# Optimization experiments

Measured on AMD Instinct MI355X. Metric: run time of the kernel, lower is better.

## Reference

```python
import jax, jax.numpy as jnp
import numpy as np

L, E, S, H, D, V = 6, 384, 256, 6, 64, 65
FF = 4 * E


def _ln(x, g, b, ddof, eps=1e-5):
    mean = jnp.mean(x, axis=-1, keepdims=True)
    var = jnp.var(x, axis=-1, keepdims=True, ddof=ddof)
    return g * (x - mean) / jnp.sqrt(var + eps) + b


def setup_inputs() -> dict:
    key = jax.random.key(0)
    ks = jax.random.split(key, 16)
    std = 0.02
    inp = {
        'x': jax.random.randint(ks[0], (64, S), 0, V),
        'tok_emb': jax.random.normal(ks[1], (V, E)) * std,
        'pos_emb': jax.random.normal(ks[2], (S, E)) * std,
        'Wq': jax.random.normal(ks[3], (L, E, H * D)) * std,
        'Wk': jax.random.normal(ks[4], (L, E, H * D)) * std,
        'Wv': jax.random.normal(ks[5], (L, E, H * D)) * std,
        'Wproj': jax.random.normal(ks[6], (L, H * D, E)) * std,
        'bproj': jnp.zeros((L, E)),
        'W1': jax.random.normal(ks[7], (L, E, FF)) * std,
        'b1': jnp.zeros((L, FF)),
        'W2': jax.random.normal(ks[8], (L, FF, E)) * std,
        'b2': jnp.zeros((L, E)),
        'ln1_g': jnp.ones((L, E)), 'ln1_b': jnp.zeros((L, E)),
        'ln2_g': jnp.ones((L, E)), 'ln2_b': jnp.zeros((L, E)),
        'lnf_g': jnp.ones((E,)), 'lnf_b': jnp.zeros((E,)),
        'Wlm': jax.random.normal(ks[9], (E, V)) * std,
        'blm': jnp.zeros((V,)),
    }
    return inp


def _forward(x, tok_emb, pos_emb, Wq, Wk, Wv, Wproj, bproj, W1, b1, W2, b2,
             ln1_g, ln1_b, ln2_g, ln2_b, lnf_g, lnf_b, Wlm, blm):
    B, T = x.shape
    h = tok_emb[x] + pos_emb[:T]  # [B,T,E]
    causal = jnp.tril(jnp.ones((T, T), dtype=bool))
    neg_inf = jnp.finfo(h.dtype).min
    for l in range(L):
        hn = _ln(h, ln1_g[l], ln1_b[l], ddof=1)  # custom LayerNorm uses unbiased var
        q = (hn @ Wq[l]).reshape(B, T, H, D)
        k = (hn @ Wk[l]).reshape(B, T, H, D)
        v = (hn @ Wv[l]).reshape(B, T, H, D)
        wei = jnp.einsum('bqhd,bkhd->bhqk', q, k) * (D ** -0.5)
        wei = jnp.where(causal, wei, neg_inf)
        wei = jax.nn.softmax(wei, axis=-1)
        att = jnp.einsum('bhqk,bkhd->bqhd', wei, v).reshape(B, T, H * D)
        h = h + att @ Wproj[l] + bproj[l]
        hn = _ln(h, ln2_g[l], ln2_b[l], ddof=1)
        h = h + jax.nn.relu(hn @ W1[l] + b1[l]) @ W2[l] + b2[l]
    h = _ln(h, lnf_g, lnf_b, ddof=0)  # nn.LayerNorm uses biased var
    return h @ Wlm + blm  # logits [B,T,V]


def reference(x, tok_emb, pos_emb, Wq, Wk, Wv, Wproj, bproj, W1, b1, W2, b2,
              ln1_g, ln1_b, ln2_g, ln2_b, lnf_g, lnf_b, Wlm, blm):
    return _forward(x, tok_emb, pos_emb, Wq, Wk, Wv, Wproj, bproj, W1, b1, W2, b2,
                    ln1_g, ln1_b, ln2_g, ln2_b, lnf_g, lnf_b, Wlm, blm)
```

## Files before the change

kernel.cpp:

```cpp
#include <hip/hip_runtime.h>

#define L_  6
#define E_  384
#define T_  256
#define H_  6
#define D_  64
#define V_  65
#define FF_ 1536
#define B_  64
#define BT_ (B_*T_)
#define HD_ 384

typedef __attribute__((ext_vector_type(8))) short short8;
typedef __attribute__((ext_vector_type(4))) float f32x4;
typedef unsigned short us;
typedef unsigned int u32;

__device__ __forceinline__ us f2bf(float f) {
  u32 u = __float_as_uint(f);
  u32 r = (u + 0x7fffu + ((u >> 16) & 1u)) >> 16;
  return (us)r;
}
__device__ __forceinline__ float bf2f(us v) {
  return __uint_as_float(((u32)v) << 16);
}

__device__ __forceinline__ int xcd_swz(int b, int nwg) {
  const int q = nwg >> 3;
  return (b & 7) * q + (b >> 3);
}

__global__ void embed_kernel(const int* __restrict__ x, const float* __restrict__ tok,
                             const float* __restrict__ pos, us* __restrict__ h) {
  const int total8 = BT_ * E_ / 8;
  for (int i = blockIdx.x * blockDim.x + threadIdx.x; i < total8;
       i += gridDim.x * blockDim.x) {
    const int flat = i << 3;
    const int row  = flat / E_;
    const int e    = flat - row * E_;
    const int id   = x[row];
    const float4 a0 = *reinterpret_cast<const float4*>(tok + id * E_ + e);
    const float4 a1 = *reinterpret_cast<const float4*>(tok + id * E_ + e + 4);
    const float4 p0 = *reinterpret_cast<const float4*>(pos + (row & (T_ - 1)) * E_ + e);
    const float4 p1 = *reinterpret_cast<const float4*>(pos + (row & (T_ - 1)) * E_ + e + 4);
    short8 o;
    o[0] = (short)f2bf(a0.x + p0.x); o[1] = (short)f2bf(a0.y + p0.y);
    o[2] = (short)f2bf(a0.z + p0.z); o[3] = (short)f2bf(a0.w + p0.w);
    o[4] = (short)f2bf(a1.x + p1.x); o[5] = (short)f2bf(a1.y + p1.y);
    o[6] = (short)f2bf(a1.z + p1.z); o[7] = (short)f2bf(a1.w + p1.w);
    *reinterpret_cast<short8*>(h + flat) = o;
  }
}

template<int DDOF>
__global__ __launch_bounds__(512)
void stats_kernel(const us* __restrict__ h, float2* __restrict__ st) {
  const int wave = threadIdx.x >> 6;
  const int lane = threadIdx.x & 63;
  const int row  = (blockIdx.x << 3) + wave;
  float sum = 0.f, sq = 0.f;
  if (lane < 48) {
    const short8 v = *reinterpret_cast<const short8*>(h + (size_t)row * E_ + lane * 8);
#pragma unroll
    for (int j = 0; j < 8; ++j) {
      const float f = bf2f((us)v[j]);
      sum += f; sq += f * f;
    }
  }
#pragma unroll
  for (int off = 32; off > 0; off >>= 1) {
    sum += __shfl_xor(sum, off);
    sq  += __shfl_xor(sq, off);
  }
  if (lane == 0) {
    const float mean = sum * (1.f / E_);
    const float var  = (sq - E_ * mean * mean) * (1.f / (E_ - DDOF));
    float2 o; o.x = mean; o.y = rsqrtf(var + 1e-5f);
    st[row] = o;
  }
}

__global__ void prep_kernel(const float* __restrict__ Wq, const float* __restrict__ Wk,
                            const float* __restrict__ Wv, const float* __restrict__ Wpr,
                            const float* __restrict__ W1, const float* __restrict__ W2,
                            const float* __restrict__ Wlm,
                            us* qkvT, us* projT, us* W1T, us* W2T, us* WlmT,
                            const float* __restrict__ ln1g,
                            const float* __restrict__ ln2g,
                            const float* __restrict__ lnfg) {
  const int t = blockIdx.x;
  const float* src; us* dst; const float* g = nullptr;
  int K, N, Ndst, bx, by;
  if (t < 2592) {
    const int z = t / 144, rem = t % 144;
    bx = rem % 12; by = rem / 12;
    const int sel = z / 6, l = z % 6;
    src = (sel == 0 ? Wq : sel == 1 ? Wk : Wv) + (size_t)l * 147456;
    dst = qkvT + (size_t)l * 442368 + sel * 147456;
    g = ln1g + l * 384; K = 384; N = 384; Ndst = 384;
  } else if (t < 3456) {
    const int t2 = t - 2592, l = t2 / 144, rem = t2 % 144;
    bx = rem % 12; by = rem / 12;
    src = Wpr + (size_t)l * 147456; dst = projT + (size_t)l * 147456;
    K = 384; N = 384; Ndst = 384;
  } else if (t < 6912) {
    const int t3 = t - 3456, l = t3 / 576, rem = t3 % 576;
    bx = rem % 48; by = rem / 48;
    src = W1 + (size_t)l * 589824; dst = W1T + (size_t)l * 589824;
    g = ln2g + l * 384; K = 384; N = 1536; Ndst = 1536;
  } else if (t < 10368) {
    const int t4 = t - 6912, l = t4 / 576, rem = t4 % 576;
    bx = rem % 12; by = rem / 12;
    src = W2 + (size_t)l * 589824; dst = W2T + (size_t)l * 589824;
    K = 1536; N = 384; Ndst = 384;
  } else {
    const int t5 = t - 10368;
    bx = t5 % 4; by = t5 / 4;
    src = Wlm; dst = WlmT; g = lnfg; K = 384; N = 65; Ndst = 128;
  }
  __shared__ float tt[32][33];
  const int n0 = bx << 5, k0 = by << 5;
  const int tx = threadIdx.x & 31, ty = threadIdx.x >> 5;
#pragma unroll
  for (int j = 0; j < 32; j += 8) {
    const int n = n0 + tx;
    tt[ty + j][tx] = (n < N) ? src[(size_t)(k0 + ty + j) * N + n] : 0.f;
  }
  __syncthreads();
  const float gk = g ? g[k0 + tx] : 1.f;
#pragma unroll
  for (int j = 0; j < 32; j += 8) {
    const int n = n0 + ty + j;
    if (n < Ndst) dst[(size_t)n * K + k0 + tx] = f2bf(tt[tx][ty + j] * gk);
  }
}

__global__ void c12_all(const float* __restrict__ Wq, const float* __restrict__ Wk,
                        const float* __restrict__ Wv, const float* __restrict__ W1,
                        const float* __restrict__ Wlm,
                        const float* __restrict__ ln1g, const float* __restrict__ ln1b,
                        const float* __restrict__ ln2g, const float* __restrict__ ln2b,
                        const float* __restrict__ lnfg, const float* __restrict__ lnfb,
                        float2* c12q, float2* c12f, float2* c12lm) {
  const int t = blockIdx.x;
  const float* Wz; const float* gz; const float* bz; float2* outb; int N, nb;
  if (t < 108) {
    const int bx = t % 6, zy = t / 6, sel = zy / 6, l = zy % 6;
    Wz = (sel == 0 ? Wq : sel == 1 ? Wk : Wv) + (size_t)l * 147456;
    gz = ln1g + l * 384; bz = ln1b + l * 384;
    outb = c12q + (size_t)l * 1152 + sel * 384; N = 384; nb = bx << 6;
  } else if (t < 252) {
    const int t2 = t - 108, bx = t2 % 24, l = t2 / 24;
    Wz = W1 + (size_t)l * 589824;
    gz = ln2g + l * 384; bz = ln2b + l * 384;
    outb = c12f + (size_t)l * 1536; N = 1536; nb = bx << 6;
  } else {
    const int bx = t - 252;
    Wz = Wlm; gz = lnfg; bz = lnfb;
    outb = c12lm; N = 65; nb = bx << 6;
  }
  __shared__ float p1[4][64], p2[4][64];
  const int tt = threadIdx.x;
  const int c = tt & 63, kq = tt >> 6;
  const int n = nb + c;
  float s1 = 0.f, s2 = 0.f;
  if (n < N) {
    for (int k = kq * 96; k < kq * 96 + 96; ++k) {
      const float w = Wz[(size_t)k * N + n];
      s1 = fmaf(gz[k], w, s1);
      s2 = fmaf(bz[k], w, s2);
    }
  }
  p1[kq][c] = s1; p2[kq][c] = s2;
  __syncthreads();
  if (tt < 64 && nb + tt < N) {
    float2 o;
    o.x = p1[0][tt] + p1[1][tt] + p1[2][tt] + p1[3][tt];
    o.y = p2[0][tt] + p2[1][tt] + p2[2][tt] + p2[3][tt];
    outb[nb + tt] = o;
  }
}

template<int ROWS, int CHPR, int NTH>
__device__ __forceinline__ void stageG(const us* g, int rowUs, us* lds, int tid) {
#pragma unroll
  for (int j = 0; j < ROWS * CHPR / NTH; ++j) {
    const int fl  = j * NTH + tid;
    const int row = fl / CHPR;
    const int c   = fl % CHPR;
    const int gc  = (CHPR == 8) ? (c ^ (row & 7)) : (c ^ ((row >> 1) & 3));
    const us* src = g + (size_t)row * rowUs + gc * 8;
    __builtin_amdgcn_global_load_lds(
        (const __attribute__((address_space(1))) u32*)src,
        (__attribute__((address_space(3))) u32*)(lds + ((fl >> 6) << 9)),
        16, 0, 0);
  }
}

#define GEMM_LOOP(K_, NT_)                                                        \
  const int NT = (NT_);                                                           \
  _Pragma("unroll")                                                               \
  for (int p = 0; p < BUFS - 1; ++p) {                                            \
    stageG<BM, 4, 256>(Abase + p * 32, (K_), As[p], tid);                         \
    stageG<BN, 4, 256>(Bbase + p * 32, (K_), Bs[p], tid);                         \
  }                                                                               \
  int cb = 0;                                                                     \
  for (int t = 0; t < NT; ++t) {                                                  \
    if constexpr (BUFS == 4) {                                                    \
      if (t < NT - 2)       asm volatile("s_waitcnt vmcnt(%0)" :: "n"(2 * LPS) : "memory"); \
      else if (t == NT - 2) asm volatile("s_waitcnt vmcnt(%0)" :: "n"(LPS) : "memory");     \
      else                  asm volatile("s_waitcnt vmcnt(0)" ::: "memory");      \
    } else {                                                                      \
      if (t < NT - 1)       asm volatile("s_waitcnt vmcnt(%0)" :: "n"(LPS) : "memory");     \
      else                  asm volatile("s_waitcnt vmcnt(0)" ::: "memory");      \
    }                                                                             \
    __builtin_amdgcn_s_barrier();                                                 \
    __builtin_amdgcn_sched_barrier(0);                                            \
    if (t + BUFS - 1 < NT) {                                                      \
      int ib = cb + (BUFS - 1); if (ib >= BUFS) ib -= BUFS;                       \
      stageG<BM, 4, 256>(Abase + (t + BUFS - 1) * 32, (K_), As[ib], tid);         \
      stageG<BN, 4, 256>(Bbase + (t + BUFS - 1) * 32, (K_), Bs[ib], tid);         \
    }                                                                             \
    short8 af[FM], bfr[FN];                                                       \
    _Pragma("unroll")                                                             \
    for (int mt = 0; mt < FM; ++mt) {                                             \
      const int row = wm + mt * 16 + fm;                                          \
      af[mt] = *(const short8*)(As[cb] + row * 32 + ((fg ^ ((row >> 1) & 3)) << 3)); \
    }                                                                             \
    _Pragma("unroll")                                                             \
    for (int nt = 0; nt < FN; ++nt) {                                             \
      const int row = wn + nt * 16 + fm;                                          \
      bfr[nt] = *(const short8*)(Bs[cb] + row * 32 + ((fg ^ ((row >> 1) & 3)) << 3)); \
    }                                                                             \
    __builtin_amdgcn_s_setprio(1);                                                \
    _Pragma("unroll")                                                             \
    for (int mt = 0; mt < FM; ++mt)                                               \
      _Pragma("unroll")                                                           \
      for (int nt = 0; nt < FN; ++nt)                                             \
        acc[mt][nt] = __builtin_amdgcn_mfma_f32_16x16x32_bf16(af[mt], bfr[nt], acc[mt][nt], 0, 0, 0); \
    __builtin_amdgcn_s_setprio(0);                                                \
    cb = (cb + 1 == BUFS) ? 0 : cb + 1;                                           \
  }

template<int FM, int FN, int BUFS>
__global__ __launch_bounds__(256)
void gemm_mfma(const us* __restrict__ A, const us* __restrict__ Bt,
               const float* __restrict__ bias, const us* Res,
               us* __restrict__ O, int N, int K, int gx) {
  constexpr int BM = FM * 32, BN = FN * 32;
  constexpr int LPS = (BM + BN) * 4 / 256;
  __shared__ us As[BUFS][BM * 32];
  __shared__ us Bs[BUFS][BN * 32];
  const int tid = threadIdx.x;
  const int lid = xcd_swz(blockIdx.x, gridDim.x);
  const int bnI = lid % gx, bmI = lid / gx;
  const int bm = bmI * BM, bn = bnI * BN;
  const int wv = tid >> 6, ln = tid & 63;
  const int fm = ln & 15, fg = ln >> 4;
  const int wm = (wv >> 1) * (FM * 16), wn = (wv & 1) * (FN * 16);
  const us* Abase = A + (size_t)bm * K;
  const us* Bbase = Bt + (size_t)bn * K;

  f32x4 acc[FM][FN];
  const f32x4 zz = {0.f, 0.f, 0.f, 0.f};
#pragma unroll
  for (int i = 0; i < FM; ++i)
#pragma unroll
    for (int j = 0; j < FN; ++j) acc[i][j] = zz;

  GEMM_LOOP(K, K >> 5)

#pragma unroll
  for (int mt = 0; mt < FM; ++mt) {
#pragma unroll
    for (int nt = 0; nt < FN; ++nt) {
      const int col  = bn + wn + nt * 16 + fm;
      const int row0 = bm + wm + mt * 16 + fg * 4;
      const float bc = bias[col];
#pragma unroll
      for (int r = 0; r < 4; ++r) {
        const size_t idx = (size_t)(row0 + r) * N + col;
        O[idx] = f2bf(acc[mt][nt][r] + bc + bf2f(Res[idx]));
      }
    }
  }
}

template<int FM, int FN, int EPI, int BUFS>
__global__ __launch_bounds__(256)
void gemm_fold(const us* __restrict__ A, const us* __restrict__ Bt,
               const float2* __restrict__ st, const float2* __restrict__ c12,
               const float* __restrict__ bias, void* O0, void* O1,
               int N, int gx) {
  constexpr int K = 384;
  constexpr int BM = FM * 32, BN = FN * 32;
  constexpr int LPS = (BM + BN) * 4 / 256;
  __shared__ us As[BUFS][BM * 32];
  __shared__ us Bs[BUFS][BN * 32];
  const int tid = threadIdx.x;
  const int lid = xcd_swz(blockIdx.x, gridDim.x);
  const int bnI = lid % gx, bmI = lid / gx;
  const int bm = bmI * BM, bn = bnI * BN;
  const int wv = tid >> 6, ln = tid & 63;
  const int fm = ln & 15, fg = ln >> 4;
  const int wm = (wv >> 1) * (FM * 16), wn = (wv & 1) * (FN * 16);
  const us* Abase = A + (size_t)bm * K;
  const us* Bbase = Bt + (size_t)bn * K;

  f32x4 acc[FM][FN];
  const f32x4 zz = {0.f, 0.f, 0.f, 0.f};
#pragma unroll
  for (int i = 0; i < FM; ++i)
#pragma unroll
    for (int j = 0; j < FN; ++j) acc[i][j] = zz;

  GEMM_LOOP(K, 12)

#pragma unroll
  for (int mt = 0; mt < FM; ++mt) {
    const int row0 = bm + wm + mt * 16 + fg * 4;
    float2 sr[4];
#pragma unroll
    for (int r = 0; r < 4; ++r) sr[r] = st[row0 + r];
#pragma unroll
    for (int nt = 0; nt < FN; ++nt) {
      const int col = bn + wn + nt * 16 + fm;
      if (EPI == 3 && col >= V_) continue;
      const float2 cc = c12[col];
      float vals[4];
#pragma unroll
      for (int r = 0; r < 4; ++r)
        vals[r] = sr[r].y * (acc[mt][nt][r] - sr[r].x * cc.x) + cc.y;
      if (EPI == 0) {
        if (col < 768) {
          us* qk = (us*)O0;
#pragma unroll
          for (int r = 0; r < 4; ++r)
            qk[(size_t)(row0 + r) * 768 + col] = f2bf(vals[r]);
        } else {
          const int d = col - 768;
          const int hh = d >> 6, dd = d & 63;
          const int bI = row0 >> 8, t0 = row0 & 255;
          us* vt = (us*)O1;
          ushort4 pk;
          pk.x = f2bf(vals[0]); pk.y = f2bf(vals[1]);
          pk.z = f2bf(vals[2]); pk.w = f2bf(vals[3]);
          *reinterpret_cast<ushort4*>(vt + ((size_t)((bI * H_ + hh) * 64 + dd)) * 256 + t0) = pk;
        }
      } else if (EPI == 2) {
        us* o = (us*)O0;
        const float bc = bias[col];
#pragma unroll
        for (int r = 0; r < 4; ++r)
          o[(size_t)(row0 + r) * N + col] = f2bf(fmaxf(vals[r] + bc, 0.f));
      } else {
        float* o = (float*)O0;
        const float bc = bias[col];
#pragma unroll
        for (int r = 0; r < 4; ++r)
          o[(size_t)(row0 + r) * V_ + col] = vals[r] + bc;
      }
    }
  }
}

__global__ __launch_bounds__(256)
void attn_mfma(const us* __restrict__ qk, const us* __restrict__ vT,
               us* __restrict__ ab) {
  __shared__ us Ks[2][64 * 64];
  __shared__ us Vs[2][64 * 64];
  __shared__ us Plds[4][16 * 72];
  const int tid = threadIdx.x, w = tid >> 6, l = tid & 63;
  const int m = l & 15, g = l >> 4;
  const int bi = xcd_swz(blockIdx.x, gridDim.x);
  const int b = bi / 12, rem = bi - b * 12, h = rem >> 1, p = rem & 1;
  const us* Kg = qk + (size_t)(b << 8) * 768 + 384 + h * 64;
  const us* Vg = vT + (size_t)(b * H_ + h) * 64 * 256;

  int cur = 0;
  const f32x4 zz = {0.f, 0.f, 0.f, 0.f};

#pragma unroll
  for (int half = 0; half < 2; ++half) {
    const int qt = half == 0 ? p : 3 - p;
    const int qrow = (b << 8) + (qt << 6) + (w << 4);

    short8 qf0, qf1;
    {
      const us* qp = qk + (size_t)(qrow + m) * 768 + h * 64 + g * 8;
      qf0 = *(const short8*)qp;
      qf1 = *(const short8*)(qp + 32);
    }
    float mrow[4], ssum[4];
    f32x4 o[4];
#pragma unroll
    for (int r = 0; r < 4; ++r) { mrow[r] = -1e30f; ssum[r] = 0.f; o[r] = zz; }

    stageG<64, 8, 256>(Kg, 768, Ks[cur], tid);
    stageG<64, 8, 256>(Vg, 256, Vs[cur], tid);
    __syncthreads();

    for (int kt = 0; kt <= qt; ++kt) {
      if (kt < qt) {
        stageG<64, 8, 256>(Kg + (size_t)(kt + 1) * 64 * 768, 768, Ks[cur ^ 1], tid);
        stageG<64, 8, 256>(Vg + (kt + 1) * 64,               256, Vs[cur ^ 1], tid);
      }
      f32x4 s[4];
      __builtin_amdgcn_s_setprio(1);
#pragma unroll
      for (int nt = 0; nt < 4; ++nt) {
        const int row = nt * 16 + m;
        const int sw  = row & 7;
        short8 kf0 = *(const short8*)(Ks[cur] + row * 64 + ((g ^ sw) << 3));
        short8 kf1 = *(const short8*)(Ks[cur] + row * 64 + (((4 | g) ^ sw) << 3));
        f32x4 z = zz;
        z = __builtin_amdgcn_mfma_f32_16x16x32_bf16(qf0, kf0, z, 0, 0, 0);
        z = __builtin_amdgcn_mfma_f32_16x16x32_bf16(qf1, kf1, z, 0, 0, 0);
        s[nt] = z;
      }
      __builtin_amdgcn_s_setprio(0);
      const bool diag = (kt == qt);
      float pr[4][4], tmax[4];
#pragma unroll
      for (int r = 0; r < 4; ++r) tmax[r] = -1e30f;
#pragma unroll
      for (int nt = 0; nt < 4; ++nt)
#pragma unroll
        for (int r = 0; r < 4; ++r) {
          float v = s[nt][r] * 0.125f;
          if (diag) {
            const int key = nt * 16 + m;
            const int qq  = (w << 4) + (g << 2) + r;
            if (key > qq) v = -1e30f;
          }
          pr[nt][r] = v;
          tmax[r] = fmaxf(tmax[r], v);
        }
#pragma unroll
      for (int xm = 1; xm < 16; xm <<= 1)
#pragma unroll
        for (int r = 0; r < 4; ++r) tmax[r] = fmaxf(tmax[r], __shfl_xor(tmax[r], xm));
      float sc[4], tsum[4];
#pragma unroll
      for (int r = 0; r < 4; ++r) {
        const float nm = fmaxf(mrow[r], tmax[r]);
        sc[r] = __expf(mrow[r] - nm);
        mrow[r] = nm;
        tsum[r] = 0.f;
      }
#pragma unroll
      for (int nt = 0; nt < 4; ++nt)
#pragma unroll
        for (int r = 0; r < 4; ++r) {
          pr[nt][r] = __expf(pr[nt][r] - mrow[r]);
          tsum[r] += pr[nt][r];
        }
#pragma unroll
      for (int xm = 1; xm < 16; xm <<= 1)
#pragma unroll
        for (int r = 0; r < 4; ++r) tsum[r] += __shfl_xor(tsum[r], xm);
#pragma unroll
      for (int r = 0; r < 4; ++r) ssum[r] = ssum[r] * sc[r] + tsum[r];
#pragma unroll
      for (int nt = 0; nt < 4; ++nt)
#pragma unroll
        for (int r = 0; r < 4; ++r) o[nt][r] *= sc[r];
#pragma unroll
      for (int nt = 0; nt < 4; ++nt)
#pragma unroll
        for (int r = 0; r < 4; ++r)
          Plds[w][(g * 4 + r) * 72 + nt * 16 + m] = f2bf(pr[nt][r]);
      __builtin_amdgcn_s_setprio(1);
#pragma unroll
      for (int kc = 0; kc < 2; ++kc) {
        short8 pa = *(const short8*)&Plds[w][m * 72 + kc * 32 + g * 8];
#pragma unroll
        for (int nd = 0; nd < 4; ++nd) {
          const int row = nd * 16 + m;
          short8 vf = *(const short8*)(Vs[cur] + row * 64 + ((((kc << 2) | g) ^ (row & 7)) << 3));
          o[nd] = __builtin_amdgcn_mfma_f32_16x16x32_bf16(pa, vf, o[nd], 0, 0, 0);
        }
      }
      __builtin_amdgcn_s_setprio(0);
      __syncthreads();
      cur ^= 1;
    }
#pragma unroll
    for (int r = 0; r < 4; ++r) {
      const float inv = 1.f / ssum[r];
      const size_t rowoff = (size_t)(qrow + g * 4 + r) * 384 + h * 64;
#pragma unroll
      for (int nd = 0; nd < 4; ++nd)
        ab[rowoff + nd * 16 + m] = f2bf(o[nd][r] * inv);
    }
  }
}

extern "C" void kernel_launch(void* const* d_in, const int* in_sizes, int n_in,
                              void* d_out, int out_size, void* d_ws, size_t ws_size,
                              hipStream_t stream) {
  const int*   x    = (const int*)  d_in[0];
  const float* tok  = (const float*)d_in[1];
  const float* pos  = (const float*)d_in[2];
  const float* Wq   = (const float*)d_in[3];
  const float* Wk   = (const float*)d_in[4];
  const float* Wv   = (const float*)d_in[5];
  const float* Wpr  = (const float*)d_in[6];
  const float* bpr  = (const float*)d_in[7];
  const float* W1   = (const float*)d_in[8];
  const float* b1   = (const float*)d_in[9];
  const float* W2   = (const float*)d_in[10];
  const float* b2   = (const float*)d_in[11];
  const float* ln1g = (const float*)d_in[12];
  const float* ln1b = (const float*)d_in[13];
  const float* ln2g = (const float*)d_in[14];
  const float* ln2b = (const float*)d_in[15];
  const float* lnfg = (const float*)d_in[16];
  const float* lnfb = (const float*)d_in[17];
  const float* Wlm  = (const float*)d_in[18];
  const float* blm  = (const float*)d_in[19];
  float* out = (float*)d_out;

  char* W = (char*)d_ws;
  us*     h    = (us*)(W + 0);
  us*     qkb  = (us*)(W + 12582912);
  us*     vTb  = (us*)(W + 37748736);
  us*     abb  = (us*)(W + 50331648);
  us*     ffa  = (us*)(W + 12582912);
  us*     qkvT = (us*)(W + 62914560);
  us*     projT= (us*)(W + 68222976);
  us*     W1T  = (us*)(W + 69992448);
  us*     W2T  = (us*)(W + 77070336);
  us*     WlmT = (us*)(W + 84148224);
  float2* st   = (float2*)(W + 84246528);
  float2* c12q = (float2*)(W + 84377600);
  float2* c12f = (float2*)(W + 84432896);
  float2* c12lm= (float2*)(W + 84506624);

  prep_kernel<<<10416, 256, 0, stream>>>(Wq, Wk, Wv, Wpr, W1, W2, Wlm,
                                         qkvT, projT, W1T, W2T, WlmT,
                                         ln1g, ln2g, lnfg);
  c12_all<<<254, 256, 0, stream>>>(Wq, Wk, Wv, W1, Wlm,
                                   ln1g, ln1b, ln2g, ln2b, lnfg, lnfb,
                                   c12q, c12f, c12lm);

  embed_kernel<<<3072, 256, 0, stream>>>(x, tok, pos, h);

  for (int l = 0; l < L_; ++l) {
    stats_kernel<1><<<BT_/8, 512, 0, stream>>>(h, st);
    gemm_fold<4,4,0,3><<<1152, 256, 0, stream>>>(
        h, qkvT + (size_t)l*442368, st, c12q + (size_t)l*1152, nullptr,
        qkb, vTb, 1152, 9);
    attn_mfma<<<B_*H_*2, 256, 0, stream>>>(qkb, vTb, abb);
    gemm_mfma<2,4,4><<<768, 256, 0, stream>>>(
        abb, projT + (size_t)l*147456, bpr + l*E_, h, h, 384, 384, 3);
    stats_kernel<1><<<BT_/8, 512, 0, stream>>>(h, st);
    gemm_fold<4,4,2,3><<<1536, 256, 0, stream>>>(
        h, W1T + (size_t)l*589824, st, c12f + (size_t)l*1536, b1 + l*FF_,
        ffa, nullptr, 1536, 12);
    gemm_mfma<2,4,4><<<768, 256, 0, stream>>>(
        ffa, W2T + (size_t)l*589824, b2 + l*E_, h, h, 384, 1536, 3);
  }

  stats_kernel<0><<<BT_/8, 512, 0, stream>>>(h, st);
  gemm_fold<2,4,3,3><<<256, 256, 0, stream>>>(
      h, WlmT, st, c12lm, blm, out, nullptr, 128, 1);
}
```

Before: 876.1 us.

## Share K/V tile loads between both query tiles in causal attention

The attention kernel used to walk the key/value tiles twice, once per query tile in its balanced pair. It now keeps both query tiles' softmax state live and walks the K/V tiles once, so each staged tile feeds both query tiles until the shorter one hits its diagonal. This cuts global K/V loads and barriers for the shorter tile, at the cost of more live registers (two sets of accumulators and running stats), which may lower occupancy.

```diff
diff --git a/kernel.cpp b/kernel.cpp
--- a/kernel.cpp
+++ b/kernel.cpp
@@ -374,125 +374,139 @@
   const int m = l & 15, g = l >> 4;
   const int bi = xcd_swz(blockIdx.x, gridDim.x);
   const int b = bi / 12, rem = bi - b * 12, h = rem >> 1, p = rem & 1;
+  const int qtA = 3 - p, qtB = p;
+  const int qrowA = (b << 8) + (qtA << 6) + (w << 4);
+  const int qrowB = (b << 8) + (qtB << 6) + (w << 4);
   const us* Kg = qk + (size_t)(b << 8) * 768 + 384 + h * 64;
   const us* Vg = vT + (size_t)(b * H_ + h) * 64 * 256;
 
+  short8 qA0, qA1, qB0, qB1;
+  {
+    const us* qp = qk + (size_t)(qrowA + m) * 768 + h * 64 + g * 8;
+    qA0 = *(const short8*)qp;
+    qA1 = *(const short8*)(qp + 32);
+    const us* qp2 = qk + (size_t)(qrowB + m) * 768 + h * 64 + g * 8;
+    qB0 = *(const short8*)qp2;
+    qB1 = *(const short8*)(qp2 + 32);
+  }
+  const f32x4 zz = {0.f, 0.f, 0.f, 0.f};
+  float mrowA[4], ssumA[4], mrowB[4], ssumB[4];
+  f32x4 oA[4], oB[4];
+#pragma unroll
+  for (int r = 0; r < 4; ++r) {
+    mrowA[r] = -1e30f; ssumA[r] = 0.f; oA[r] = zz;
+    mrowB[r] = -1e30f; ssumB[r] = 0.f; oB[r] = zz;
+  }
+
   int cur = 0;
-  const f32x4 zz = {0.f, 0.f, 0.f, 0.f};
-
-#pragma unroll
-  for (int half = 0; half < 2; ++half) {
-    const int qt = half == 0 ? p : 3 - p;
-    const int qrow = (b << 8) + (qt << 6) + (w << 4);
-
-    short8 qf0, qf1;
-    {
-      const us* qp = qk + (size_t)(qrow + m) * 768 + h * 64 + g * 8;
-      qf0 = *(const short8*)qp;
-      qf1 = *(const short8*)(qp + 32);
-    }
-    float mrow[4], ssum[4];
-    f32x4 o[4];
-#pragma unroll
-    for (int r = 0; r < 4; ++r) { mrow[r] = -1e30f; ssum[r] = 0.f; o[r] = zz; }
-
-    stageG<64, 8, 256>(Kg, 768, Ks[cur], tid);
-    stageG<64, 8, 256>(Vg, 256, Vs[cur], tid);
+  stageG<64, 8, 256>(Kg, 768, Ks[0], tid);
+  stageG<64, 8, 256>(Vg, 256, Vs[0], tid);
+  __syncthreads();
+
+  auto step = [&](const short8& qf0, const short8& qf1, float* mrow,
+                  float* ssum, f32x4* o, bool diag) {
+    f32x4 s[4];
+    __builtin_amdgcn_s_setprio(1);
+#pragma unroll
+    for (int nt = 0; nt < 4; ++nt) {
+      const int row = nt * 16 + m;
+      const int sw  = row & 7;
+      short8 kf0 = *(const short8*)(Ks[cur] + row * 64 + ((g ^ sw) << 3));
+      short8 kf1 = *(const short8*)(Ks[cur] + row * 64 + (((4 | g) ^ sw) << 3));
+      f32x4 z = zz;
+      z = __builtin_amdgcn_mfma_f32_16x16x32_bf16(qf0, kf0, z, 0, 0, 0);
+      z = __builtin_amdgcn_mfma_f32_16x16x32_bf16(qf1, kf1, z, 0, 0, 0);
+      s[nt] = z;
+    }
+    __builtin_amdgcn_s_setprio(0);
+    float pr[4][4], tmax[4];
+#pragma unroll
+    for (int r = 0; r < 4; ++r) tmax[r] = -1e30f;
+#pragma unroll
+    for (int nt = 0; nt < 4; ++nt)
+#pragma unroll
+      for (int r = 0; r < 4; ++r) {
+        float v = s[nt][r] * 0.125f;
+        if (diag) {
+          const int key = nt * 16 + m;
+          const int qq  = (w << 4) + (g << 2) + r;
+          if (key > qq) v = -1e30f;
+        }
+        pr[nt][r] = v;
+        tmax[r] = fmaxf(tmax[r], v);
+      }
+#pragma unroll
+    for (int xm = 1; xm < 16; xm <<= 1)
+#pragma unroll
+      for (int r = 0; r < 4; ++r) tmax[r] = fmaxf(tmax[r], __shfl_xor(tmax[r], xm));
+    float sc[4], tsum[4];
+#pragma unroll
+    for (int r = 0; r < 4; ++r) {
+      const float nm = fmaxf(mrow[r], tmax[r]);
+      sc[r] = __expf(mrow[r] - nm);
+      mrow[r] = nm;
+      tsum[r] = 0.f;
+    }
+#pragma unroll
+    for (int nt = 0; nt < 4; ++nt)
+#pragma unroll
+      for (int r = 0; r < 4; ++r) {
+        pr[nt][r] = __expf(pr[nt][r] - mrow[r]);
+        tsum[r] += pr[nt][r];
+      }
+#pragma unroll
+    for (int xm = 1; xm < 16; xm <<= 1)
+#pragma unroll
+      for (int r = 0; r < 4; ++r) tsum[r] += __shfl_xor(tsum[r], xm);
+#pragma unroll
+    for (int r = 0; r < 4; ++r) ssum[r] = ssum[r] * sc[r] + tsum[r];
+#pragma unroll
+    for (int nt = 0; nt < 4; ++nt)
+#pragma unroll
+      for (int r = 0; r < 4; ++r) o[nt][r] *= sc[r];
+#pragma unroll
+    for (int nt = 0; nt < 4; ++nt)
+#pragma unroll
+      for (int r = 0; r < 4; ++r)
+        Plds[w][(g * 4 + r) * 72 + nt * 16 + m] = f2bf(pr[nt][r]);
+    __builtin_amdgcn_s_setprio(1);
+#pragma unroll
+    for (int kc = 0; kc < 2; ++kc) {
+      short8 pa = *(const short8*)&Plds[w][m * 72 + kc * 32 + g * 8];
+#pragma unroll
+      for (int nd = 0; nd < 4; ++nd) {
+        const int row = nd * 16 + m;
+        short8 vf = *(const short8*)(Vs[cur] + row * 64 + ((((kc << 2) | g) ^ (row & 7)) << 3));
+        o[nd] = __builtin_amdgcn_mfma_f32_16x16x32_bf16(pa, vf, o[nd], 0, 0, 0);
+      }
+    }
+    __builtin_amdgcn_s_setprio(0);
+  };
+
+  for (int kt = 0; kt <= qtA; ++kt) {
+    if (kt < qtA) {
+      stageG<64, 8, 256>(Kg + (size_t)(kt + 1) * 64 * 768, 768, Ks[cur ^ 1], tid);
+      stageG<64, 8, 256>(Vg + (kt + 1) * 64,               256, Vs[cur ^ 1], tid);
+    }
+    step(qA0, qA1, mrowA, ssumA, oA, kt == qtA);
+    if (kt <= qtB)
+      step(qB0, qB1, mrowB, ssumB, oB, kt == qtB);
     __syncthreads();
-
-    for (int kt = 0; kt <= qt; ++kt) {
-      if (kt < qt) {
-        stageG<64, 8, 256>(Kg + (size_t)(kt + 1) * 64 * 768, 768, Ks[cur ^ 1], tid);
-        stageG<64, 8, 256>(Vg + (kt + 1) * 64,               256, Vs[cur ^ 1], tid);
-      }
-      f32x4 s[4];
-      __builtin_amdgcn_s_setprio(1);
-#pragma unroll
-      for (int nt = 0; nt < 4; ++nt) {
-        const int row = nt * 16 + m;
-        const int sw  = row & 7;
-        short8 kf0 = *(const short8*)(Ks[cur] + row * 64 + ((g ^ sw) << 3));
-        short8 kf1 = *(const short8*)(Ks[cur] + row * 64 + (((4 | g) ^ sw) << 3));
-        f32x4 z = zz;
-        z = __builtin_amdgcn_mfma_f32_16x16x32_bf16(qf0, kf0, z, 0, 0, 0);
-        z = __builtin_amdgcn_mfma_f32_16x16x32_bf16(qf1, kf1, z, 0, 0, 0);
-        s[nt] = z;
-      }
-      __builtin_amdgcn_s_setprio(0);
-      const bool diag = (kt == qt);
-      float pr[4][4], tmax[4];
-#pragma unroll
-      for (int r = 0; r < 4; ++r) tmax[r] = -1e30f;
-#pragma unroll
-      for (int nt = 0; nt < 4; ++nt)
-#pragma unroll
-        for (int r = 0; r < 4; ++r) {
-          float v = s[nt][r] * 0.125f;
-          if (diag) {
-            const int key = nt * 16 + m;
-            const int qq  = (w << 4) + (g << 2) + r;
-            if (key > qq) v = -1e30f;
-          }
-          pr[nt][r] = v;
-          tmax[r] = fmaxf(tmax[r], v);
-        }
-#pragma unroll
-      for (int xm = 1; xm < 16; xm <<= 1)
-#pragma unroll
-        for (int r = 0; r < 4; ++r) tmax[r] = fmaxf(tmax[r], __shfl_xor(tmax[r], xm));
-      float sc[4], tsum[4];
-#pragma unroll
-      for (int r = 0; r < 4; ++r) {
-        const float nm = fmaxf(mrow[r], tmax[r]);
-        sc[r] = __expf(mrow[r] - nm);
-        mrow[r] = nm;
-        tsum[r] = 0.f;
-      }
-#pragma unroll
-      for (int nt = 0; nt < 4; ++nt)
-#pragma unroll
-        for (int r = 0; r < 4; ++r) {
-          pr[nt][r] = __expf(pr[nt][r] - mrow[r]);
-          tsum[r] += pr[nt][r];
-        }
-#pragma unroll
-      for (int xm = 1; xm < 16; xm <<= 1)
-#pragma unroll
-        for (int r = 0; r < 4; ++r) tsum[r] += __shfl_xor(tsum[r], xm);
-#pragma unroll
-      for (int r = 0; r < 4; ++r) ssum[r] = ssum[r] * sc[r] + tsum[r];
-#pragma unroll
-      for (int nt = 0; nt < 4; ++nt)
-#pragma unroll
-        for (int r = 0; r < 4; ++r) o[nt][r] *= sc[r];
-#pragma unroll
-      for (int nt = 0; nt < 4; ++nt)
-#pragma unroll
-        for (int r = 0; r < 4; ++r)
-          Plds[w][(g * 4 + r) * 72 + nt * 16 + m] = f2bf(pr[nt][r]);
-      __builtin_amdgcn_s_setprio(1);
-#pragma unroll
-      for (int kc = 0; kc < 2; ++kc) {
-        short8 pa = *(const short8*)&Plds[w][m * 72 + kc * 32 + g * 8];
-#pragma unroll
-        for (int nd = 0; nd < 4; ++nd) {
-          const int row = nd * 16 + m;
-          short8 vf = *(const short8*)(Vs[cur] + row * 64 + ((((kc << 2) | g) ^ (row & 7)) << 3));
-          o[nd] = __builtin_amdgcn_mfma_f32_16x16x32_bf16(pa, vf, o[nd], 0, 0, 0);
-        }
-      }
-      __builtin_amdgcn_s_setprio(0);
-      __syncthreads();
-      cur ^= 1;
-    }
-#pragma unroll
-    for (int r = 0; r < 4; ++r) {
-      const float inv = 1.f / ssum[r];
-      const size_t rowoff = (size_t)(qrow + g * 4 + r) * 384 + h * 64;
-#pragma unroll
-      for (int nd = 0; nd < 4; ++nd)
-        ab[rowoff + nd * 16 + m] = f2bf(o[nd][r] * inv);
-    }
+    cur ^= 1;
+  }
+
+#pragma unroll
+  for (int r = 0; r < 4; ++r) {
+    const float invA = 1.f / ssumA[r];
+    const size_t roA = (size_t)(qrowA + g * 4 + r) * 384 + h * 64;
+#pragma unroll
+    for (int nd = 0; nd < 4; ++nd)
+      ab[roA + nd * 16 + m] = f2bf(oA[nd][r] * invA);
+    const float invB = 1.f / ssumB[r];
+    const size_t roB = (size_t)(qrowB + g * 4 + r) * 384 + h * 64;
+#pragma unroll
+    for (int nd = 0; nd < 4; ++nd)
+      ab[roB + nd * 16 + m] = f2bf(oB[nd][r] * invB);
   }
 }
 
```

Result: no change. 887.0 us (+1.2%).
